# Performance work log

Hardware: AMD Instinct MI355X
Metric: run time of the kernel (lower is better)

Reference implementation:

```python
import jax, jax.numpy as jnp
import numpy as np

BALL_BBOX_SIZE = 40.0
PLAYER_DS = 16
BALL_DS = 4
MAX_DET = 100
B, HP, WP = 64, 68, 120
HB, WB = 272, 480


def _nms2d(x):
    # keep only local maxima in a 3x3 window (kornia-style NonMaximaSuppression2d)
    m = jax.lax.reduce_window(x, -jnp.inf, jax.lax.max, (1, 1, 3, 3), (1, 1, 1, 1), 'SAME')
    return jnp.where(x == m, x, jnp.zeros((), x.dtype))


def _detect_from_map(conf_logits, ds, max_det, bbox_map):
    # conf_logits: [B,2,h,w]; bbox_map: [B,4,h,w] or None
    p = jax.nn.softmax(conf_logits, axis=1)          # softmax applied in forward() for 'detect' phase
    conf = _nms2d(p)[:, 1]                           # [B,h,w], positive-class channel
    bsz, h, w = conf.shape
    flat = conf.reshape(bsz, h * w)
    values, indices = jax.lax.top_k(flat, max_det)   # == full descending sort truncated to max_det
    fds = jnp.float32(ds)
    xc = (indices % w).astype(jnp.float32) * fds + (fds - 1.0) / 2.0
    yc = (indices // w).astype(jnp.float32) * fds + (fds - 1.0) / 2.0
    if bbox_map is None:
        # ball: fixed-size boxes, zero center offsets
        temp = jnp.zeros((bsz, 4, max_det), jnp.float32).at[:, 2:4].set(BALL_BBOX_SIZE)
    else:
        # offsets/sizes are fractions of image size -> scale to pixels, then gather per top-k cell
        scale = jnp.array([w * ds, h * ds, w * ds, h * ds], jnp.float32).reshape(1, 4, 1)
        bm = bbox_map.reshape(bsz, 4, h * w) * scale
        temp = jnp.take_along_axis(bm, indices[:, None, :], axis=2)  # [B,4,max_det]
    bx = xc + temp[:, 0]
    by = yc + temp[:, 1]
    return jnp.stack([bx - 0.5 * temp[:, 2],
                      by - 0.5 * temp[:, 3],
                      bx + 0.5 * temp[:, 2],
                      by + 0.5 * temp[:, 3],
                      values], axis=-1)              # [B,max_det,5] = x1,y1,x2,y2,score


def setup_inputs() -> dict:
    key = jax.random.key(0)
    k1, k2, k3 = jax.random.split(key, 3)
    return {
        'player_feature_map': jax.random.normal(k1, (B, 2, HP, WP), jnp.float32),
        'player_bbox': jax.random.normal(k2, (B, 4, HP, WP), jnp.float32) * 0.05,
        'ball_feature_map': jax.random.normal(k3, (B, 2, HB, WB), jnp.float32),
    }


def reference(player_feature_map, player_bbox, ball_feature_map):
    player_det = _detect_from_map(player_feature_map, PLAYER_DS, MAX_DET, player_bbox)
    ball_det = _detect_from_map(ball_feature_map, BALL_DS, MAX_DET, None)
    return (player_det, ball_det)
```

## Files before the change

kernel.cpp:

```cpp
#include <hip/hip_runtime.h>
#include <stdint.h>
#include <math.h>

#define TPB   512
#define KTOP  100
#define K1    128
#define KSLOT 192
#define CAP   768
#define SR    8

#define HB 272
#define WB 480
#define NSB 34
#define HP 68
#define WP 120
#define NSP 9
#define NB 64

__device__ __forceinline__ float G_exact(float D) {
    float t = -fabsf(D);
    float etf = (float)exp((double)t);
    return (D > 0.0f) ? __fdiv_rn(1.0f, __fadd_rn(etf, 1.0f))
                      : __fdiv_rn(etf, __fadd_rn(1.0f, etf));
}

__device__ __forceinline__ uint32_t flip_f32(float D) {
    uint32_t u = __float_as_uint(D);
    return (u & 0x80000000u) ? ~u : (u | 0x80000000u);
}

__device__ __forceinline__ void suffix_scan_256(uint32_t* hist) {
    if (threadIdx.x < 64) {
        int lane = threadIdx.x;
        uint32_t h0 = hist[4*lane+0], h1 = hist[4*lane+1];
        uint32_t h2 = hist[4*lane+2], h3 = hist[4*lane+3];
        uint32_t tot = h0 + h1 + h2 + h3;
        uint32_t run = tot;
        #pragma unroll
        for (int d = 1; d < 64; d <<= 1) {
            uint32_t o = __shfl_down(run, d, 64);
            if (lane + d < 64) run += o;
        }
        uint32_t ab = run - tot;
        hist[4*lane+3] = ab + h3;
        hist[4*lane+2] = ab + h3 + h2;
        hist[4*lane+1] = ab + h3 + h2 + h1;
        hist[4*lane+0] = ab + tot;
    }
    __syncthreads();
}

__device__ void bitonic_sort_256(uint64_t* keys) {
    for (int k = 2; k <= 256; k <<= 1) {
        for (int j = k >> 1; j > 0; j >>= 1) {
            int i = threadIdx.x;
            if (i < 256) {
                int ixj = i ^ j;
                if (ixj > i) {
                    uint64_t ka = keys[i], kb = keys[ixj];
                    bool sw = ((ka < kb) == ((i & k) == 0));
                    if (sw) { keys[i] = kb; keys[ixj] = ka; }
                }
            }
            __syncthreads();
        }
    }
}

template<int W>
__device__ __forceinline__ void row6(const float* df, int row, int c4, float* a) {
    const float4 m = ((const float4*)df)[(row * W + c4) >> 2];
    a[1] = m.x; a[2] = m.y; a[3] = m.z; a[4] = m.w;
    a[0] = (c4 > 0)     ? df[row * W + c4 - 1] : -INFINITY;
    a[5] = (c4 + 4 < W) ? df[row * W + c4 + 4] : -INFINITY;
}

template<int H, int W, int NS>
__device__ __forceinline__ void stage1_impl(const float* __restrict__ x,
                                            int s, int b,
                                            uint32_t* __restrict__ key_out,
                                            unsigned char* smem)
{
    constexpr int W4 = W / 4;
    constexpr int tileRows = SR + 2;
    const int r0 = s * SR;
    const int rows = (H - r0 < SR) ? (H - r0) : SR;

    float*    df   = (float*)smem;
    uint32_t* surv = (uint32_t*)(df + tileRows * W);
    uint32_t* hist = surv + CAP;
    uint32_t* outb = hist + 256;
    __shared__ int s_cnt, s_out;
    __shared__ uint32_t s_bin, s_ab, s_bin2, s_none;
    if (threadIdx.x == 0) { s_cnt = 0; s_out = 0; s_none = 0; }
    if (threadIdx.x < 256) hist[threadIdx.x] = 0;

    const float*  x0  = x + (size_t)b * 2 * H * W;
    const float*  x1  = x0 + (size_t)H * W;
    const float4* x0v = (const float4*)x0;
    const float4* x1v = (const float4*)x1;
    float4* dfv = (float4*)df;

    constexpr int nt4 = tileRows * W4;
    for (int t = threadIdx.x; t < nt4; t += TPB) {
        int tr = t / W4, c4 = t - tr * W4;
        int r = r0 - 1 + tr;
        float4 d4 = make_float4(-INFINITY, -INFINITY, -INFINITY, -INFINITY);
        if (r >= 0 && r < H) {
            float4 a = x0v[r * W4 + c4];
            float4 c = x1v[r * W4 + c4];
            d4.x = __fsub_rn(c.x, a.x);
            d4.y = __fsub_rn(c.y, a.y);
            d4.z = __fsub_rn(c.z, a.z);
            d4.w = __fsub_rn(c.w, a.w);
        }
        dfv[t] = d4;
    }
    __syncthreads();

    const int groups = rows * W4;
    for (int g = threadIdx.x; g < groups; g += TPB) {
        int lr = g / W4, c4 = (g - lr * W4) << 2;
        int tr = lr + 1;
        float ap[6], ac[6], an[6];
        row6<W>(df, tr - 1, c4, ap);
        row6<W>(df, tr,     c4, ac);
        row6<W>(df, tr + 1, c4, an);
        #pragma unroll
        for (int j = 0; j < 4; ++j) {
            float v = ac[j + 1];
            float mx = fmaxf(fmaxf(fmaxf(ap[j], ap[j+1]), fmaxf(ap[j+2], an[j])),
                             fmaxf(fmaxf(an[j+1], an[j+2]), fmaxf(ac[j], ac[j+2])));
            bool keep;
            if (v >= mx) keep = true;
            else if (mx - v >= 0.25f && mx < 13.0f) keep = false;
            else keep = (G_exact(v) == G_exact(mx));
            if (keep) {
                uint32_t key16 = flip_f32(v) >> 16;
                int pos = atomicAdd(&s_cnt, 1);
                if (pos < CAP)
                    surv[pos] = (key16 << 16) | ((uint32_t)lr << 9) | (uint32_t)(c4 + j);
                atomicAdd(&hist[key16 >> 8], 1u);
            }
        }
    }
    __syncthreads();
    const int n = (s_cnt < CAP) ? s_cnt : CAP;

    suffix_scan_256(hist);
    if (threadIdx.x < 256) {
        uint32_t si = hist[threadIdx.x];
        uint32_t sn = (threadIdx.x < 255) ? hist[threadIdx.x + 1] : 0u;
        if (threadIdx.x == 0 && si < K1) s_none = 1;
        if (si >= K1 && sn < K1) { s_bin = threadIdx.x; s_ab = sn; }
    }
    __syncthreads();

    uint32_t T16 = 0;
    if (!s_none) {
        const uint32_t b3 = s_bin;
        const uint32_t k2 = K1 - s_ab;
        if (threadIdx.x < 256) hist[threadIdx.x] = 0;
        __syncthreads();
        for (int t = threadIdx.x; t < n; t += TPB) {
            uint32_t sv = surv[t];
            if ((sv >> 24) == b3) atomicAdd(&hist[(sv >> 16) & 255u], 1u);
        }
        __syncthreads();
        suffix_scan_256(hist);
        if (threadIdx.x < 256) {
            uint32_t si = hist[threadIdx.x];
            uint32_t sn = (threadIdx.x < 255) ? hist[threadIdx.x + 1] : 0u;
            if (si >= k2 && sn < k2) s_bin2 = threadIdx.x;
        }
        __syncthreads();
        T16 = (b3 << 8) | s_bin2;
    }

    if (threadIdx.x < KSLOT) outb[threadIdx.x] = 0;
    __syncthreads();
    for (int t = threadIdx.x; t < n; t += TPB) {
        uint32_t sv = surv[t];
        if ((sv >> 16) >= T16) {
            int pos = atomicAdd(&s_out, 1);
            if (pos < KSLOT) outb[pos] = sv;
        }
    }
    __syncthreads();
    if (threadIdx.x < KSLOT)
        key_out[((size_t)b * NS + s) * KSLOT + threadIdx.x] = outb[threadIdx.x];
}

__global__ __launch_bounds__(TPB) void stage1(const float* __restrict__ bmap,
                                              const float* __restrict__ pmap,
                                              uint32_t* __restrict__ bkey,
                                              uint32_t* __restrict__ pkey)
{
    extern __shared__ unsigned char smem[];
    if (blockIdx.x < NSB)
        stage1_impl<HB, WB, NSB>(bmap, blockIdx.x, blockIdx.y, bkey, smem);
    else
        stage1_impl<HP, WP, NSP>(pmap, blockIdx.x - NSB, blockIdx.y, pkey, smem);
}

template<int H, int W, int NS, bool BALL>
__device__ __forceinline__ void stage2_impl(const float* __restrict__ xmap,
                                            const float* __restrict__ pbbox,
                                            const uint32_t* __restrict__ key_in,
                                            float* __restrict__ outp,
                                            int b, unsigned char* smem)
{
    constexpr int M = NS * KSLOT;
    const float* x0 = xmap + (size_t)b * 2 * H * W;
    const float* x1 = x0 + (size_t)H * W;
    const uint32_t* kin = key_in + (size_t)b * M;

    uint32_t* keys = (uint32_t*)smem;
    uint32_t* hist = keys + M;
    uint64_t* outb = (uint64_t*)(hist + 256);
    __shared__ int s_out;
    __shared__ uint32_t s_bin, s_ab, s_bin2, s_none;
    if (threadIdx.x == 0) { s_out = 0; s_none = 0; }
    if (threadIdx.x < 256) hist[threadIdx.x] = 0;
    __syncthreads();

    for (int t = threadIdx.x; t < M; t += TPB) {
        uint32_t k = kin[t];
        keys[t] = k;
        if (k) atomicAdd(&hist[k >> 24], 1u);
    }
    __syncthreads();
    suffix_scan_256(hist);
    if (threadIdx.x < 256) {
        uint32_t si = hist[threadIdx.x];
        uint32_t sn = (threadIdx.x < 255) ? hist[threadIdx.x + 1] : 0u;
        if (threadIdx.x == 0 && si < K1) s_none = 1;
        if (si >= K1 && sn < K1) { s_bin = threadIdx.x; s_ab = sn; }
    }
    __syncthreads();

    uint32_t T16 = 0;
    if (!s_none) {
        const uint32_t b3 = s_bin;
        const uint32_t k2 = K1 - s_ab;
        if (threadIdx.x < 256) hist[threadIdx.x] = 0;
        __syncthreads();
        for (int t = threadIdx.x; t < M; t += TPB) {
            uint32_t k = keys[t];
            if (k && (k >> 24) == b3) atomicAdd(&hist[(k >> 16) & 255u], 1u);
        }
        __syncthreads();
        suffix_scan_256(hist);
        if (threadIdx.x < 256) {
            uint32_t si = hist[threadIdx.x];
            uint32_t sn = (threadIdx.x < 255) ? hist[threadIdx.x + 1] : 0u;
            if (si >= k2 && sn < k2) s_bin2 = threadIdx.x;
        }
        __syncthreads();
        T16 = (b3 << 8) | s_bin2;
    }

    if (threadIdx.x < 256) outb[threadIdx.x] = 0;
    __syncthreads();
    for (int t = threadIdx.x; t < M; t += TPB) {
        uint32_t k = keys[t];
        if (k && (k >> 16) >= T16) {
            int pos = atomicAdd(&s_out, 1);
            if (pos < 256) {
                int sIdx = t / KSLOT;
                int lr = (k >> 9) & 7, c = k & 511;
                int gidx = (sIdx * SR + lr) * W + c;
                float D = __fsub_rn(x1[gidx], x0[gidx]);
                float p = G_exact(D);
                outb[pos] = ((uint64_t)__float_as_uint(p) << 32) | (uint32_t)(~gidx);
            }
        }
    }
    __syncthreads();
    bitonic_sort_256(outb);

    if (threadIdx.x < KTOP) {
        uint64_t k = outb[threadIdx.x];
        int id = (int)(~(uint32_t)k);
        float o0 = 0.f, o1 = 0.f, o2 = 0.f, o3 = 0.f, val = 0.f;
        if ((unsigned)id < (unsigned)(H * W)) {
            val = __uint_as_float((uint32_t)(k >> 32));
            int yy = id / W, xx = id - yy * W;
            constexpr float ds = BALL ? 4.0f : 16.0f;
            float xc = (float)xx * ds + (ds - 1.0f) * 0.5f;
            float yc = (float)yy * ds + (ds - 1.0f) * 0.5f;
            float t0 = 0.f, t1 = 0.f;
            float t2 = BALL ? 40.0f : 0.0f, t3 = BALL ? 40.0f : 0.0f;
            if (!BALL) {
                const float* bb = pbbox + (size_t)b * 4 * H * W;
                constexpr float sx = (float)W * ds, sy = (float)H * ds;
                t0 = bb[id]             * sx;
                t1 = bb[id + H * W]     * sy;
                t2 = bb[id + 2 * H * W] * sx;
                t3 = bb[id + 3 * H * W] * sy;
            }
            float bx = xc + t0, by = yc + t1;
            o0 = bx - 0.5f * t2;
            o1 = by - 0.5f * t3;
            o2 = bx + 0.5f * t2;
            o3 = by + 0.5f * t3;
        }
        float* op = outp + (size_t)threadIdx.x * 5;
        op[0] = o0; op[1] = o1; op[2] = o2; op[3] = o3; op[4] = val;
    }
}

__global__ __launch_bounds__(TPB) void stage2(const float* __restrict__ bmap,
                                              const float* __restrict__ pmap,
                                              const float* __restrict__ pbbox,
                                              const uint32_t* __restrict__ bkey,
                                              const uint32_t* __restrict__ pkey,
                                              float* __restrict__ out)
{
    extern __shared__ unsigned char smem[];
    if (blockIdx.x < NB) {
        int b = blockIdx.x;
        stage2_impl<HB, WB, NSB, true>(bmap, nullptr, bkey,
            out + (size_t)NB * KTOP * 5 + (size_t)b * KTOP * 5, b, smem);
    } else {
        int b = blockIdx.x - NB;
        stage2_impl<HP, WP, NSP, false>(pmap, pbbox, pkey,
            out + (size_t)b * KTOP * 5, b, smem);
    }
}

extern "C" void kernel_launch(void* const* d_in, const int* in_sizes, int n_in,
                              void* d_out, int out_size, void* d_ws, size_t ws_size,
                              hipStream_t stream) {
    const float* pmap  = (const float*)d_in[0];
    const float* pbbox = (const float*)d_in[1];
    const float* bmap  = (const float*)d_in[2];
    float* out = (float*)d_out;

    uint32_t* ws_bkey = (uint32_t*)d_ws;
    uint32_t* ws_pkey = ws_bkey + (size_t)NB * NSB * KSLOT;

    size_t lds1 = (size_t)(SR + 2) * WB * 4 + (size_t)CAP * 4 + 1024 + (size_t)KSLOT * 4;
    stage1<<<dim3(NSB + NSP, NB), TPB, lds1, stream>>>(bmap, pmap, ws_bkey, ws_pkey);

    size_t lds2 = (size_t)NSB * KSLOT * 4 + 1024 + 2048;
    stage2<<<2 * NB, TPB, lds2, stream>>>(bmap, pmap, pbbox, ws_bkey, ws_pkey, out);
}
```

Before: 140.5 us.

## Use wave-aggregated atomics and rank-based selection instead of bitonic sort

Replaces per-thread shared-memory atomics for compaction and histogramming with wave-level ballot aggregation, which cuts atomic contention on the shared counters. Replaces the 256-element bitonic sort, with its many barriers, by a rank computation in which each key counts the larger keys and is scattered straight to its output slot. Stage-1 global loads are batched into registers before the subtraction to raise memory-level parallelism. The output buffer is now zeroed first and then scattered into, which adds extra global writes and an ordering dependence between those writes within the block.

```diff
diff --git a/kernel.cpp b/kernel.cpp
--- a/kernel.cpp
+++ b/kernel.cpp
@@ -27,6 +27,32 @@
 __device__ __forceinline__ uint32_t flip_f32(float D) {
     uint32_t u = __float_as_uint(D);
     return (u & 0x80000000u) ? ~u : (u | 0x80000000u);
+}
+
+__device__ __forceinline__ int agg_push(int* ctr, bool active) {
+    uint64_t m = __ballot(active);
+    int pos = -1;
+    if (active) {
+        int lane = threadIdx.x & 63;
+        int lead = __ffsll((unsigned long long)m) - 1;
+        int before = (int)__popcll(m & ((1ull << lane) - 1ull));
+        int base = 0;
+        if (lane == lead) base = atomicAdd(ctr, (int)__popcll(m));
+        base = __shfl(base, lead, 64);
+        pos = base + before;
+    }
+    return pos;
+}
+
+__device__ __forceinline__ void hist_clustered(uint32_t* hist, uint32_t bin, bool active) {
+    uint64_t todo = __ballot(active);
+    while (todo) {
+        int lead = __ffsll((unsigned long long)todo) - 1;
+        uint32_t b = (uint32_t)__shfl((int)bin, lead, 64);
+        uint64_t same = __ballot(active && (bin == b));
+        if ((int)(threadIdx.x & 63) == lead) atomicAdd(&hist[b], (uint32_t)__popcll(same));
+        todo &= ~same;
+    }
 }
 
 __device__ __forceinline__ void suffix_scan_256(uint32_t* hist) {
@@ -50,23 +76,6 @@
     __syncthreads();
 }
 
-__device__ void bitonic_sort_256(uint64_t* keys) {
-    for (int k = 2; k <= 256; k <<= 1) {
-        for (int j = k >> 1; j > 0; j >>= 1) {
-            int i = threadIdx.x;
-            if (i < 256) {
-                int ixj = i ^ j;
-                if (ixj > i) {
-                    uint64_t ka = keys[i], kb = keys[ixj];
-                    bool sw = ((ka < kb) == ((i & k) == 0));
-                    if (sw) { keys[i] = kb; keys[ixj] = ka; }
-                }
-            }
-            __syncthreads();
-        }
-    }
-}
-
 template<int W>
 __device__ __forceinline__ void row6(const float* df, int row, int c4, float* a) {
     const float4 m = ((const float4*)df)[(row * W + c4) >> 2];
@@ -102,19 +111,37 @@
     float4* dfv = (float4*)df;
 
     constexpr int nt4 = tileRows * W4;
-    for (int t = threadIdx.x; t < nt4; t += TPB) {
-        int tr = t / W4, c4 = t - tr * W4;
-        int r = r0 - 1 + tr;
-        float4 d4 = make_float4(-INFINITY, -INFINITY, -INFINITY, -INFINITY);
-        if (r >= 0 && r < H) {
-            float4 a = x0v[r * W4 + c4];
-            float4 c = x1v[r * W4 + c4];
-            d4.x = __fsub_rn(c.x, a.x);
-            d4.y = __fsub_rn(c.y, a.y);
-            d4.z = __fsub_rn(c.z, a.z);
-            d4.w = __fsub_rn(c.w, a.w);
-        }
-        dfv[t] = d4;
+    constexpr int NCH = (nt4 + TPB - 1) / TPB;
+    {
+        float4 ra[NCH], rc[NCH];
+        #pragma unroll
+        for (int u = 0; u < NCH; ++u) {
+            int t = threadIdx.x + u * TPB;
+            if (t < nt4) {
+                int tr = t / W4, c4 = t - tr * W4;
+                int r = r0 - 1 + tr;
+                if (r >= 0 && r < H) {
+                    ra[u] = x0v[r * W4 + c4];
+                    rc[u] = x1v[r * W4 + c4];
+                } else {
+                    ra[u] = make_float4(0.f, 0.f, 0.f, 0.f);
+                    rc[u] = make_float4(-INFINITY, -INFINITY, -INFINITY, -INFINITY);
+                }
+            }
+        }
+        #pragma unroll
+        for (int u = 0; u < NCH; ++u) {
+            int t = threadIdx.x + u * TPB;
+            if (t < nt4) {
+                float4 a = ra[u], c = rc[u];
+                float4 d4;
+                d4.x = __fsub_rn(c.x, a.x);
+                d4.y = __fsub_rn(c.y, a.y);
+                d4.z = __fsub_rn(c.z, a.z);
+                d4.w = __fsub_rn(c.w, a.w);
+                dfv[t] = d4;
+            }
+        }
     }
     __syncthreads();
 
@@ -135,13 +162,11 @@
             if (v >= mx) keep = true;
             else if (mx - v >= 0.25f && mx < 13.0f) keep = false;
             else keep = (G_exact(v) == G_exact(mx));
-            if (keep) {
-                uint32_t key16 = flip_f32(v) >> 16;
-                int pos = atomicAdd(&s_cnt, 1);
-                if (pos < CAP)
-                    surv[pos] = (key16 << 16) | ((uint32_t)lr << 9) | (uint32_t)(c4 + j);
-                atomicAdd(&hist[key16 >> 8], 1u);
-            }
+            uint32_t key16 = flip_f32(v) >> 16;
+            int pos = agg_push(&s_cnt, keep);
+            if (keep && pos < CAP)
+                surv[pos] = (key16 << 16) | ((uint32_t)lr << 9) | (uint32_t)(c4 + j);
+            hist_clustered(hist, key16 >> 8, keep);
         }
     }
     __syncthreads();
@@ -181,10 +206,9 @@
     __syncthreads();
     for (int t = threadIdx.x; t < n; t += TPB) {
         uint32_t sv = surv[t];
-        if ((sv >> 16) >= T16) {
-            int pos = atomicAdd(&s_out, 1);
-            if (pos < KSLOT) outb[pos] = sv;
-        }
+        bool take = ((sv >> 16) >= T16);
+        int pos = agg_push(&s_out, take);
+        if (take && pos < KSLOT) outb[pos] = sv;
     }
     __syncthreads();
     if (threadIdx.x < KSLOT)
@@ -222,12 +246,14 @@
     __shared__ uint32_t s_bin, s_ab, s_bin2, s_none;
     if (threadIdx.x == 0) { s_out = 0; s_none = 0; }
     if (threadIdx.x < 256) hist[threadIdx.x] = 0;
+
+    for (int t = threadIdx.x; t < KTOP * 5; t += TPB) outp[t] = 0.f;
     __syncthreads();
 
     for (int t = threadIdx.x; t < M; t += TPB) {
         uint32_t k = kin[t];
         keys[t] = k;
-        if (k) atomicAdd(&hist[k >> 24], 1u);
+        hist_clustered(hist, k >> 24, k != 0);
     }
     __syncthreads();
     suffix_scan_256(hist);
@@ -260,31 +286,41 @@
         T16 = (b3 << 8) | s_bin2;
     }
 
-    if (threadIdx.x < 256) outb[threadIdx.x] = 0;
+    if (threadIdx.x < 256) { outb[threadIdx.x] = 0; hist[threadIdx.x] = 0; }
     __syncthreads();
     for (int t = threadIdx.x; t < M; t += TPB) {
         uint32_t k = keys[t];
-        if (k && (k >> 16) >= T16) {
-            int pos = atomicAdd(&s_out, 1);
-            if (pos < 256) {
-                int sIdx = t / KSLOT;
-                int lr = (k >> 9) & 7, c = k & 511;
-                int gidx = (sIdx * SR + lr) * W + c;
-                float D = __fsub_rn(x1[gidx], x0[gidx]);
-                float p = G_exact(D);
-                outb[pos] = ((uint64_t)__float_as_uint(p) << 32) | (uint32_t)(~gidx);
-            }
-        }
-    }
-    __syncthreads();
-    bitonic_sort_256(outb);
-
-    if (threadIdx.x < KTOP) {
+        bool take = (k != 0) && ((k >> 16) >= T16);
+        int pos = agg_push(&s_out, take);
+        if (take && pos < 256) {
+            int sIdx = t / KSLOT;
+            int lr = (k >> 9) & 7, c = k & 511;
+            int gidx = (sIdx * SR + lr) * W + c;
+            float D = __fsub_rn(x1[gidx], x0[gidx]);
+            float p = G_exact(D);
+            outb[pos] = ((uint64_t)__float_as_uint(p) << 32) | (uint32_t)(~gidx);
+        }
+    }
+    __syncthreads();
+
+    {
+        int i = threadIdx.x & 255;
+        int half = threadIdx.x >> 8;
+        uint64_t ki = outb[i];
+        uint32_t cnt = 0;
+        int j0 = half * 128;
+        #pragma unroll 4
+        for (int j = j0; j < j0 + 128; ++j) cnt += (outb[j] > ki) ? 1u : 0u;
+        atomicAdd(&hist[i], cnt);
+    }
+    __syncthreads();
+
+    if (threadIdx.x < 256) {
         uint64_t k = outb[threadIdx.x];
-        int id = (int)(~(uint32_t)k);
-        float o0 = 0.f, o1 = 0.f, o2 = 0.f, o3 = 0.f, val = 0.f;
-        if ((unsigned)id < (unsigned)(H * W)) {
-            val = __uint_as_float((uint32_t)(k >> 32));
+        uint32_t r = hist[threadIdx.x];
+        if (k != 0 && r < KTOP) {
+            int id = (int)(~(uint32_t)k);
+            float val = __uint_as_float((uint32_t)(k >> 32));
             int yy = id / W, xx = id - yy * W;
             constexpr float ds = BALL ? 4.0f : 16.0f;
             float xc = (float)xx * ds + (ds - 1.0f) * 0.5f;
@@ -300,13 +336,13 @@
                 t3 = bb[id + 3 * H * W] * sy;
             }
             float bx = xc + t0, by = yc + t1;
-            o0 = bx - 0.5f * t2;
-            o1 = by - 0.5f * t3;
-            o2 = bx + 0.5f * t2;
-            o3 = by + 0.5f * t3;
-        }
-        float* op = outp + (size_t)threadIdx.x * 5;
-        op[0] = o0; op[1] = o1; op[2] = o2; op[3] = o3; op[4] = val;
+            float* op = outp + (size_t)r * 5;
+            op[0] = bx - 0.5f * t2;
+            op[1] = by - 0.5f * t3;
+            op[2] = bx + 0.5f * t2;
+            op[3] = by + 0.5f * t3;
+            op[4] = val;
+        }
     }
 }
 
```

Measured after the change: 147.1 us. 1.05x slower.
